# Performance work log

Hardware: AMD Instinct MI355X
Metric: run time of the kernel (lower is better)

The kernel has to match this reference:

```python
import jax, jax.numpy as jnp
import numpy as np

D_MODEL = 1024
N_HEAD = 16
DK = D_MODEL // N_HEAD
D_FF = 2048
EPS = 1e-6
NEG = -1e10


def layer_norm(x, gamma, beta):
    # torch .std() is unbiased (N-1), and eps is added to std (not var)
    mean = jnp.mean(x, axis=-1, keepdims=True)
    var = jnp.sum((x - mean) ** 2, axis=-1, keepdims=True) / (x.shape[-1] - 1)
    std = jnp.sqrt(var)
    return gamma * (x - mean) / (std + EPS) + beta


def setup_inputs() -> dict:
    key = jax.random.key(0)
    ks = jax.random.split(key, 12)
    s = 0.02
    inp = {
        'x': jax.random.normal(ks[0], (16, 512, D_MODEL), dtype=jnp.float32),
        'x_mask': jax.random.randint(ks[1], (16, 1, 1, 512), 0, 2, dtype=jnp.int32),
        'Wq': jax.random.normal(ks[2], (D_MODEL, D_MODEL), dtype=jnp.float32) * s,
        'bq': jnp.zeros((D_MODEL,), jnp.float32),
        'Wk': jax.random.normal(ks[3], (D_MODEL, D_MODEL), dtype=jnp.float32) * s,
        'bk': jnp.zeros((D_MODEL,), jnp.float32),
        'Wv': jax.random.normal(ks[4], (D_MODEL, D_MODEL), dtype=jnp.float32) * s,
        'bv': jnp.zeros((D_MODEL,), jnp.float32),
        'Wo': jax.random.normal(ks[5], (D_MODEL, D_MODEL), dtype=jnp.float32) * s,
        'bo': jnp.zeros((D_MODEL,), jnp.float32),
        'gamma1': jnp.ones((D_MODEL,), jnp.float32),
        'beta1': jnp.zeros((D_MODEL,), jnp.float32),
        'W1': jax.random.normal(ks[6], (D_MODEL, D_FF), dtype=jnp.float32) * s,
        'b1': jnp.zeros((D_FF,), jnp.float32),
        'W2': jax.random.normal(ks[7], (D_FF, D_MODEL), dtype=jnp.float32) * s,
        'b2': jnp.zeros((D_MODEL,), jnp.float32),
        'gamma2': jnp.ones((D_MODEL,), jnp.float32),
        'beta2': jnp.zeros((D_MODEL,), jnp.float32),
    }
    return inp


def reference(x, x_mask, Wq, bq, Wk, bk, Wv, bv, Wo, bo, gamma1, beta1,
              W1, b1, W2, b2, gamma2, beta2):
    B, S, _ = x.shape
    # QKV projections -> [B, S, H, DK]
    q = (x @ Wq + bq).reshape(B, S, N_HEAD, DK)
    k = (x @ Wk + bk).reshape(B, S, N_HEAD, DK)
    v = (x @ Wv + bv).reshape(B, S, N_HEAD, DK)
    # scores [B, H, Sq, Sk]
    scores = jnp.einsum('bqhd,bkhd->bhqk', q, k) / jnp.sqrt(jnp.float32(DK))
    scores = jnp.where(x_mask == 0, jnp.float32(NEG), scores)
    probs = jax.nn.softmax(scores, axis=-1)
    attn = jnp.einsum('bhqk,bkhd->bqhd', probs, v).reshape(B, S, D_MODEL)
    attn_out = attn @ Wo + bo
    # residual + post-LN 1
    h = layer_norm(attn_out + x, gamma1, beta1)
    # FFN (exact GELU as torch nn.GELU default)
    ffn = jax.nn.gelu(h @ W1 + b1, approximate=False) @ W2 + b2
    out = layer_norm(ffn + h, gamma2, beta2)
    return out
```

## Files before the change

### kernel.cpp

```cpp
#include <hip/hip_runtime.h>
#include <math.h>

#define B_ 16
#define S_ 512
#define DM 1024
#define NH 16
#define DFF 2048

typedef short bf16x8 __attribute__((ext_vector_type(8)));
typedef float f32x4 __attribute__((ext_vector_type(4)));
typedef unsigned short u16;

__device__ __forceinline__ u16 f2bf(float f) {
  unsigned int u = __float_as_uint(f);
  u += 0x7FFF + ((u >> 16) & 1);
  return (u16)(u >> 16);
}

__device__ __forceinline__ float gelu_exact(float x) {
  return 0.5f * x * (1.0f + erff(x * 0.70710678118654752f));
}

__device__ __forceinline__ void gload_lds16(const void* g, void* l) {
  __builtin_amdgcn_global_load_lds((const __attribute__((address_space(1))) void*)g,
                                   (__attribute__((address_space(3))) void*)l, 16, 0, 0);
}


__global__ void cvt_bf16_k(const float* __restrict__ in, u16* __restrict__ out, int n) {
  int i = (blockIdx.x * blockDim.x + threadIdx.x) * 4;
  float4 v = *(const float4*)(in + i);
  uint2 pk;
  pk.x = (unsigned)f2bf(v.x) | ((unsigned)f2bf(v.y) << 16);
  pk.y = (unsigned)f2bf(v.z) | ((unsigned)f2bf(v.w) << 16);
  *(uint2*)(out + i) = pk;
}

__global__ void transpose_bf16(const float* __restrict__ W, u16* __restrict__ Wt, int K, int N) {
  __shared__ float tile[32][33];
  int n0 = blockIdx.x * 32, k0 = blockIdx.y * 32;
  int tx = threadIdx.x, ty = threadIdx.y;
#pragma unroll
  for (int j = 0; j < 32; j += 8)
    tile[ty + j][tx] = W[(size_t)(k0 + ty + j) * N + n0 + tx];
  __syncthreads();
#pragma unroll
  for (int j = 0; j < 32; j += 8)
    Wt[(size_t)(n0 + ty + j) * K + k0 + tx] = f2bf(tile[tx][ty + j]);
}

__global__ void bias_cat(const float* __restrict__ bq, const float* __restrict__ bk,
                         const float* __restrict__ bv, float* __restrict__ o) {
  int i = blockIdx.x * 256 + threadIdx.x;
  o[i] = (i < 1024) ? bq[i] : ((i < 2048) ? bk[i - 1024] : bv[i - 2048]);
}

template <int EPI>
__global__ __launch_bounds__(256, 2)
void gemm_mfma(const u16* __restrict__ A, const u16* __restrict__ Bt,
               const float* __restrict__ bias, void* __restrict__ Cout,
               u16* __restrict__ vT, int M, int N, int K) {
  __shared__ __align__(16) char lds[73728];
  const int tid = threadIdx.x;
  const int w = tid >> 6, lane = tid & 63;
  const int wm = w >> 1, wn = w & 1;

  const int gx = gridDim.x;
  const int nwg = gx * gridDim.y;
  const int lin = blockIdx.y * gx + blockIdx.x;
  const int wg = (lin & 7) * (nwg >> 3) + (lin >> 3);
  const int bm = wg / gx, bn = wg % gx;

  const int NT = K >> 5;

  const int srow = w * 16 + (lane >> 2);
  const int skel = ((lane & 3) ^ (lane >> 4)) * 8;
  const u16* gA = A + (size_t)(bm * 256 + srow) * K + skel;
  const u16* gB = Bt + (size_t)(bn * 128 + srow) * K + skel;
  const size_t rs64 = (size_t)64 * K;
  const int dstb = w * 1024;

  const int lr = lane & 15, kg = lane >> 4;
  const int kslot = (kg ^ ((lr >> 2) & 3)) << 4;
  const int fAoff = (wm * 128 + lr) * 64 + kslot;
  const int fBoff = 16384 + (wn * 64 + lr) * 64 + kslot;

  f32x4 acc[8][4];
#pragma unroll
  for (int i = 0; i < 8; ++i)
#pragma unroll
    for (int j = 0; j < 4; ++j) acc[i][j] = (f32x4){0.f, 0.f, 0.f, 0.f};

#define STAGE_A(t_, sl_)                                         \
  do {                                                           \
    const u16* g_ = gA + (size_t)(t_) * 32;                      \
    char* d_ = lds + (sl_) * 24576 + dstb;                       \
    gload_lds16(g_, d_);                                         \
    gload_lds16(g_ + rs64, d_ + 4096);                           \
    gload_lds16(g_ + 2 * rs64, d_ + 8192);                       \
    gload_lds16(g_ + 3 * rs64, d_ + 12288);                      \
  } while (0)
#define STAGE_B(t_, sl_)                                         \
  do {                                                           \
    const u16* g_ = gB + (size_t)(t_) * 32;                      \
    char* d_ = lds + (sl_) * 24576 + 16384 + dstb;               \
    gload_lds16(g_, d_);                                         \
    gload_lds16(g_ + rs64, d_ + 4096);                           \
  } while (0)

  STAGE_A(0, 0);
  STAGE_B(0, 0);
  STAGE_A(1, 1);
  STAGE_B(1, 1);
  asm volatile("s_waitcnt vmcnt(6)" ::: "memory");
  __builtin_amdgcn_s_barrier();
  __builtin_amdgcn_sched_barrier(0);

  int cs = 0, ss = 2;
  for (int t = 0; t < NT; ++t) {
    const int st = (t + 2 < NT) ? (t + 2) : (NT - 1);
    const char* fA = lds + cs * 24576 + fAoff;
    const char* fB = lds + cs * 24576 + fBoff;
    bf16x8 av[4], bv[4];
#pragma unroll
    for (int mi = 0; mi < 4; ++mi) av[mi] = *(const bf16x8*)(fA + mi * 1024);
#pragma unroll
    for (int ni = 0; ni < 4; ++ni) bv[ni] = *(const bf16x8*)(fB + ni * 1024);
    STAGE_A(st, ss);
    __builtin_amdgcn_s_barrier();
    asm volatile("s_waitcnt lgkmcnt(0)" ::: "memory");
    __builtin_amdgcn_sched_barrier(0);
    __builtin_amdgcn_s_setprio(1);
#pragma unroll
    for (int mi = 0; mi < 4; ++mi)
#pragma unroll
      for (int ni = 0; ni < 4; ++ni)
        acc[mi][ni] = __builtin_amdgcn_mfma_f32_16x16x32_bf16(av[mi], bv[ni], acc[mi][ni], 0, 0, 0);
    __builtin_amdgcn_s_setprio(0);
    __builtin_amdgcn_s_barrier();
    __builtin_amdgcn_sched_barrier(0);
#pragma unroll
    for (int mi = 0; mi < 4; ++mi) av[mi] = *(const bf16x8*)(fA + 4096 + mi * 1024);
    STAGE_B(st, ss);
    __builtin_amdgcn_s_barrier();
    asm volatile("s_waitcnt lgkmcnt(0)" ::: "memory");
    __builtin_amdgcn_sched_barrier(0);
    __builtin_amdgcn_s_setprio(1);
#pragma unroll
    for (int mi = 0; mi < 4; ++mi)
#pragma unroll
      for (int ni = 0; ni < 4; ++ni)
        acc[4 + mi][ni] = __builtin_amdgcn_mfma_f32_16x16x32_bf16(av[mi], bv[ni], acc[4 + mi][ni], 0, 0, 0);
    __builtin_amdgcn_s_setprio(0);
    asm volatile("s_waitcnt vmcnt(6)" ::: "memory");
    __builtin_amdgcn_s_barrier();
    __builtin_amdgcn_sched_barrier(0);
    cs = (cs == 2) ? 0 : cs + 1;
    ss = (ss == 2) ? 0 : ss + 1;
  }
#undef STAGE_A
#undef STAGE_B

  const int crow0 = bm * 256 + wm * 128;
  const int ccol0 = bn * 128 + wn * 64;
#pragma unroll
  for (int mi = 0; mi < 8; ++mi) {
#pragma unroll
    for (int ni = 0; ni < 4; ++ni) {
      const int col = ccol0 + ni * 16 + lr;
      const float bv = bias[col];
      const int rowb = crow0 + mi * 16 + (lane >> 4) * 4;
      float v[4];
#pragma unroll
      for (int r = 0; r < 4; ++r) v[r] = acc[mi][ni][r] + bv;
      if (EPI == 1) {
#pragma unroll
        for (int r = 0; r < 4; ++r)
          ((u16*)Cout)[(size_t)(rowb + r) * N + col] = f2bf(gelu_exact(v[r]));
      } else if (EPI == 2) {
#pragma unroll
        for (int r = 0; r < 4; ++r)
          ((float*)Cout)[(size_t)(rowb + r) * N + col] = v[r];
      } else {
        if (col < 2048) {
#pragma unroll
          for (int r = 0; r < 4; ++r)
            ((u16*)Cout)[(size_t)(rowb + r) * 2048 + col] = f2bf(v[r]);
        } else {
          const int b = rowb >> 9, s = rowb & 511;
          const int hd = col - 2048;
          ushort4 pk;
          pk.x = f2bf(v[0]); pk.y = f2bf(v[1]); pk.z = f2bf(v[2]); pk.w = f2bf(v[3]);
          *(ushort4*)(vT + ((size_t)(b * NH + (hd >> 6)) * 64 + (hd & 63)) * S_ + s) = pk;
        }
      }
    }
  }
}

__global__ __launch_bounds__(256, 3)
void attn_kernel(const u16* __restrict__ qk,
                 const u16* __restrict__ vT,
                 const int* __restrict__ mask,
                 u16* __restrict__ out) {
  __shared__ __align__(16) u16 Qs[32 * 72];
  __shared__ __align__(16) u16 Pl[32 * 520];
  __shared__ int Ml[512];
  __shared__ __align__(16) float Rmax[32][4];
  __shared__ __align__(16) float Rsum[32][4];

  const int tid = threadIdx.x;
  const int w = tid >> 6, lane = tid & 63;
  const int bid = blockIdx.x;
  const int widx = (bid & 7) * 512 + (bid >> 3);
  const int qt = widx & 15, h = (widx >> 4) & 15, b = widx >> 8;
  const int q0 = qt * 32;
  const int arow = lane & 15, kg = lane >> 4;

  {
    int r = tid >> 3, slot = tid & 7;
    bf16x8 v = *(const bf16x8*)(qk + (size_t)(b * S_ + q0 + r) * 2048 + h * 64 + slot * 8);
    *(bf16x8*)((char*)Qs + r * 144 + slot * 16) = v;
  }
  Ml[tid] = mask[b * S_ + tid];
  Ml[tid + 256] = mask[b * S_ + tid + 256];
  __syncthreads();

  f32x4 s0[8], s1[8];
  {
    bf16x8 af[2][2];
#pragma unroll
    for (int mi = 0; mi < 2; ++mi)
#pragma unroll
      for (int kk = 0; kk < 2; ++kk)
        af[mi][kk] = *(const bf16x8*)((char*)Qs + (mi * 16 + arow) * 144 + kk * 64 + kg * 16);
    const u16* kbase = qk + (size_t)(b * S_) * 2048 + 1024 + h * 64;
#pragma unroll
    for (int ni = 0; ni < 8; ++ni) {
      const int colg = w * 128 + ni * 16 + arow;
      const u16* kr = kbase + (size_t)colg * 2048 + kg * 8;
      bf16x8 bk0 = *(const bf16x8*)(kr);
      bf16x8 bk1 = *(const bf16x8*)(kr + 32);
      f32x4 a0 = {0.f, 0.f, 0.f, 0.f}, a1 = {0.f, 0.f, 0.f, 0.f};
      a0 = __builtin_amdgcn_mfma_f32_16x16x32_bf16(af[0][0], bk0, a0, 0, 0, 0);
      a0 = __builtin_amdgcn_mfma_f32_16x16x32_bf16(af[0][1], bk1, a0, 0, 0, 0);
      a1 = __builtin_amdgcn_mfma_f32_16x16x32_bf16(af[1][0], bk0, a1, 0, 0, 0);
      a1 = __builtin_amdgcn_mfma_f32_16x16x32_bf16(af[1][1], bk1, a1, 0, 0, 0);
      const bool msk = (Ml[colg] == 0);
#pragma unroll
      for (int r = 0; r < 4; ++r) {
        s0[ni][r] = msk ? -1e10f : a0[r] * 0.125f;
        s1[ni][r] = msk ? -1e10f : a1[r] * 0.125f;
      }
    }
  }

  float m0[4], m1[4];
#pragma unroll
  for (int r = 0; r < 4; ++r) {
    float a = fmaxf(fmaxf(s0[0][r], s0[1][r]), fmaxf(s0[2][r], s0[3][r]));
    float c = fmaxf(fmaxf(s0[4][r], s0[5][r]), fmaxf(s0[6][r], s0[7][r]));
    m0[r] = fmaxf(a, c);
    a = fmaxf(fmaxf(s1[0][r], s1[1][r]), fmaxf(s1[2][r], s1[3][r]));
    c = fmaxf(fmaxf(s1[4][r], s1[5][r]), fmaxf(s1[6][r], s1[7][r]));
    m1[r] = fmaxf(a, c);
  }
#pragma unroll
  for (int d = 1; d < 16; d <<= 1) {
#pragma unroll
    for (int r = 0; r < 4; ++r) {
      m0[r] = fmaxf(m0[r], __shfl_xor(m0[r], d));
      m1[r] = fmaxf(m1[r], __shfl_xor(m1[r], d));
    }
  }
  if (arow == 0) {
#pragma unroll
    for (int r = 0; r < 4; ++r) {
      Rmax[kg * 4 + r][w] = m0[r];
      Rmax[16 + kg * 4 + r][w] = m1[r];
    }
  }
  __syncthreads();
  float fm0[4], fm1[4];
#pragma unroll
  for (int r = 0; r < 4; ++r) {
    f32x4 v = *(const f32x4*)&Rmax[kg * 4 + r][0];
    fm0[r] = fmaxf(fmaxf(v[0], v[1]), fmaxf(v[2], v[3]));
    v = *(const f32x4*)&Rmax[16 + kg * 4 + r][0];
    fm1[r] = fmaxf(fmaxf(v[0], v[1]), fmaxf(v[2], v[3]));
  }

  float t0[4] = {0.f, 0.f, 0.f, 0.f}, t1[4] = {0.f, 0.f, 0.f, 0.f};
#pragma unroll
  for (int ni = 0; ni < 8; ++ni) {
#pragma unroll
    for (int r = 0; r < 4; ++r) {
      s0[ni][r] = __expf(s0[ni][r] - fm0[r]);
      t0[r] += s0[ni][r];
      s1[ni][r] = __expf(s1[ni][r] - fm1[r]);
      t1[r] += s1[ni][r];
    }
  }
#pragma unroll
  for (int ni = 0; ni < 8; ++ni) {
    const int colg = w * 128 + ni * 16 + arow;
#pragma unroll
    for (int r = 0; r < 4; ++r) {
      Pl[(kg * 4 + r) * 520 + colg] = f2bf(s0[ni][r]);
      Pl[(16 + kg * 4 + r) * 520 + colg] = f2bf(s1[ni][r]);
    }
  }
#pragma unroll
  for (int d = 1; d < 16; d <<= 1) {
#pragma unroll
    for (int r = 0; r < 4; ++r) {
      t0[r] += __shfl_xor(t0[r], d);
      t1[r] += __shfl_xor(t1[r], d);
    }
  }
  if (arow == 0) {
#pragma unroll
    for (int r = 0; r < 4; ++r) {
      Rsum[kg * 4 + r][w] = t0[r];
      Rsum[16 + kg * 4 + r][w] = t1[r];
    }
  }
  __syncthreads();

  {
    f32x4 oa[2];
    oa[0] = (f32x4){0.f, 0.f, 0.f, 0.f};
    oa[1] = (f32x4){0.f, 0.f, 0.f, 0.f};
    const u16* vb = vT + ((size_t)(b * NH + h) * 64 + w * 16 + arow) * S_ + kg * 8;
#pragma unroll
    for (int t16 = 0; t16 < 16; ++t16) {
      const int sk0 = t16 * 32;
      bf16x8 bfr = *(const bf16x8*)(vb + sk0);
#pragma unroll
      for (int mi = 0; mi < 2; ++mi) {
        bf16x8 pa = *(const bf16x8*)(Pl + (mi * 16 + arow) * 520 + sk0 + kg * 8);
        oa[mi] = __builtin_amdgcn_mfma_f32_16x16x32_bf16(pa, bfr, oa[mi], 0, 0, 0);
      }
    }
#pragma unroll
    for (int mi = 0; mi < 2; ++mi)
#pragma unroll
      for (int r = 0; r < 4; ++r) {
        const int rloc = mi * 16 + kg * 4 + r;
        f32x4 sv = *(const f32x4*)&Rsum[rloc][0];
        const float inv = 1.0f / (sv[0] + sv[1] + sv[2] + sv[3]);
        const int qrow = q0 + rloc;
        out[(size_t)(b * S_ + qrow) * DM + h * 64 + w * 16 + arow] = f2bf(oa[mi][r] * inv);
      }
  }
}

__global__ __launch_bounds__(256)
void ln_kernel(const float* __restrict__ a, const float* __restrict__ res,
               const float* __restrict__ gamma, const float* __restrict__ beta,
               float* __restrict__ out, u16* __restrict__ outb) {
  const int row = blockIdx.x, tid = threadIdx.x;
  const int w = tid >> 6, lane = tid & 63;
  const size_t base = (size_t)row * DM + tid * 4;
  float4 va = *(const float4*)(a + base);
  float4 vr = *(const float4*)(res + base);
  float v0 = va.x + vr.x, v1 = va.y + vr.y, v2 = va.z + vr.z, v3 = va.w + vr.w;
  float s = v0 + v1 + v2 + v3;
  float ss = v0 * v0 + v1 * v1 + v2 * v2 + v3 * v3;
#pragma unroll
  for (int off = 32; off >= 1; off >>= 1) {
    s += __shfl_down(s, off);
    ss += __shfl_down(ss, off);
  }
  __shared__ float ps[4], pss[4], mb[2];
  if (lane == 0) { ps[w] = s; pss[w] = ss; }
  __syncthreads();
  if (tid == 0) {
    float S = ps[0] + ps[1] + ps[2] + ps[3];
    float SS = pss[0] + pss[1] + pss[2] + pss[3];
    float mean = S * (1.0f / DM);
    float var = (SS - (float)DM * mean * mean) * (1.0f / (DM - 1));
    var = fmaxf(var, 0.f);
    mb[0] = mean;
    mb[1] = 1.0f / (sqrtf(var) + 1e-6f);
  }
  __syncthreads();
  const float mean = mb[0], rinv = mb[1];
  const int c = tid * 4;
  float y0 = gamma[c] * (v0 - mean) * rinv + beta[c];
  float y1 = gamma[c + 1] * (v1 - mean) * rinv + beta[c + 1];
  float y2 = gamma[c + 2] * (v2 - mean) * rinv + beta[c + 2];
  float y3 = gamma[c + 3] * (v3 - mean) * rinv + beta[c + 3];
  float4 o = {y0, y1, y2, y3};
  *(float4*)(out + base) = o;
  if (outb) {
    uint2 pk;
    pk.x = (unsigned)f2bf(y0) | ((unsigned)f2bf(y1) << 16);
    pk.y = (unsigned)f2bf(y2) | ((unsigned)f2bf(y3) << 16);
    *(uint2*)(outb + base) = pk;
  }
}


extern "C" void kernel_launch(void* const* d_in, const int* in_sizes, int n_in,
                              void* d_out, int out_size, void* d_ws, size_t ws_size,
                              hipStream_t stream) {
  const float* x = (const float*)d_in[0];
  const int* xm = (const int*)d_in[1];
  const float* Wq = (const float*)d_in[2];
  const float* bq = (const float*)d_in[3];
  const float* Wk = (const float*)d_in[4];
  const float* bk = (const float*)d_in[5];
  const float* Wv = (const float*)d_in[6];
  const float* bv = (const float*)d_in[7];
  const float* Wo = (const float*)d_in[8];
  const float* bo = (const float*)d_in[9];
  const float* g1 = (const float*)d_in[10];
  const float* be1 = (const float*)d_in[11];
  const float* W1 = (const float*)d_in[12];
  const float* b1 = (const float*)d_in[13];
  const float* W2 = (const float*)d_in[14];
  const float* b2 = (const float*)d_in[15];
  const float* g2 = (const float*)d_in[16];
  const float* be2 = (const float*)d_in[17];

  char* ws = (char*)d_ws;
  u16* xb = (u16*)(ws);
  u16* wqkvt = (u16*)(ws + 16777216);
  u16* wot = (u16*)(ws + 23068672);
  u16* w1t = (u16*)(ws + 25165824);
  u16* w2t = (u16*)(ws + 29360128);
  float* bqkv = (float*)(ws + 33554432);
  u16* qkb = (u16*)(ws + 33566720);
  u16* vtb = (u16*)(ws + 67121152);
  u16* attnb = (u16*)(ws + 83898368);
  float* f32a = (float*)(ws + 100675584);
  float* hbuf = (float*)(ws + 134230016);
  u16* hb = xb;

  cvt_bf16_k<<<dim3(8192), dim3(256), 0, stream>>>(x, xb, 8388608);
  transpose_bf16<<<dim3(32, 32), dim3(32, 8), 0, stream>>>(Wq, wqkvt, 1024, 1024);
  transpose_bf16<<<dim3(32, 32), dim3(32, 8), 0, stream>>>(Wk, wqkvt + 1024 * 1024, 1024, 1024);
  transpose_bf16<<<dim3(32, 32), dim3(32, 8), 0, stream>>>(Wv, wqkvt + 2 * 1024 * 1024, 1024, 1024);
  transpose_bf16<<<dim3(32, 32), dim3(32, 8), 0, stream>>>(Wo, wot, 1024, 1024);
  transpose_bf16<<<dim3(64, 32), dim3(32, 8), 0, stream>>>(W1, w1t, 1024, 2048);
  transpose_bf16<<<dim3(32, 64), dim3(32, 8), 0, stream>>>(W2, w2t, 2048, 1024);
  bias_cat<<<dim3(12), dim3(256), 0, stream>>>(bq, bk, bv, bqkv);

  gemm_mfma<3><<<dim3(24, 32), dim3(256), 0, stream>>>(xb, wqkvt, bqkv, (void*)qkb, vtb, 8192, 3072, 1024);
  attn_kernel<<<dim3(4096), dim3(256), 0, stream>>>(qkb, vtb, xm, attnb);
  gemm_mfma<2><<<dim3(8, 32), dim3(256), 0, stream>>>(attnb, wot, bo, (void*)f32a, (u16*)nullptr, 8192, 1024, 1024);
  ln_kernel<<<dim3(8192), dim3(256), 0, stream>>>(f32a, x, g1, be1, hbuf, hb);
  gemm_mfma<1><<<dim3(16, 32), dim3(256), 0, stream>>>(hb, w1t, b1, (void*)qkb, (u16*)nullptr, 8192, 2048, 1024);
  gemm_mfma<2><<<dim3(8, 32), dim3(256), 0, stream>>>(qkb, w2t, b2, (void*)f32a, (u16*)nullptr, 8192, 1024, 2048);
  ln_kernel<<<dim3(8192), dim3(256), 0, stream>>>(f32a, hbuf, g2, be2, (float*)d_out, (u16*)nullptr);
}
```

Measured before the change: 322.8 us.

## Transpose score MFMA, fold softmax scale into Q, use exp2 and packed bf16 stores

```diff
diff --git a/kernel.cpp b/kernel.cpp
--- a/kernel.cpp
+++ b/kernel.cpp
@@ -17,6 +17,12 @@
   return (u16)(u >> 16);
 }
 
+__device__ __forceinline__ unsigned cvtpk_bf16(float lo, float hi) {
+  unsigned r;
+  asm("v_cvt_pk_bf16_f32 %0, %1, %2" : "=v"(r) : "v"(lo), "v"(hi));
+  return r;
+}
+
 __device__ __forceinline__ float gelu_exact(float x) {
   return 0.5f * x * (1.0f + erff(x * 0.70710678118654752f));
 }
@@ -25,6 +31,9 @@
   __builtin_amdgcn_global_load_lds((const __attribute__((address_space(1))) void*)g,
                                    (__attribute__((address_space(3))) void*)l, 16, 0, 0);
 }
+
+#define QSCALE 0.18033688011112042f
+#define MASKNEG -1.442695e10f
 
 
 __global__ void cvt_bf16_k(const float* __restrict__ in, u16* __restrict__ out, int n) {
@@ -183,9 +192,10 @@
           ((float*)Cout)[(size_t)(rowb + r) * N + col] = v[r];
       } else {
         if (col < 2048) {
+          const float sc = (col < 1024) ? QSCALE : 1.0f;
 #pragma unroll
           for (int r = 0; r < 4; ++r)
-            ((u16*)Cout)[(size_t)(rowb + r) * 2048 + col] = f2bf(v[r]);
+            ((u16*)Cout)[(size_t)(rowb + r) * 2048 + col] = f2bf(v[r] * sc);
         } else {
           const int b = rowb >> 9, s = rowb & 511;
           const int hd = col - 2048;
@@ -205,7 +215,7 @@
                  u16* __restrict__ out) {
   __shared__ __align__(16) u16 Qs[32 * 72];
   __shared__ __align__(16) u16 Pl[32 * 520];
-  __shared__ int Ml[512];
+  __shared__ __align__(16) float Mlf[512];
   __shared__ __align__(16) float Rmax[32][4];
   __shared__ __align__(16) float Rsum[32][4];
 
@@ -222,18 +232,21 @@
     bf16x8 v = *(const bf16x8*)(qk + (size_t)(b * S_ + q0 + r) * 2048 + h * 64 + slot * 8);
     *(bf16x8*)((char*)Qs + r * 144 + slot * 16) = v;
   }
-  Ml[tid] = mask[b * S_ + tid];
-  Ml[tid + 256] = mask[b * S_ + tid + 256];
-  __syncthreads();
+  Mlf[tid] = (mask[b * S_ + tid] == 0) ? MASKNEG : 0.f;
+  Mlf[tid + 256] = (mask[b * S_ + tid + 256] == 0) ? MASKNEG : 0.f;
+  __syncthreads();
+
+  bf16x8 qf[2][2];
+#pragma unroll
+  for (int mi = 0; mi < 2; ++mi)
+#pragma unroll
+    for (int kk = 0; kk < 2; ++kk)
+      qf[mi][kk] = *(const bf16x8*)((char*)Qs + (mi * 16 + arow) * 144 + kk * 64 + kg * 16);
 
   f32x4 s0[8], s1[8];
+  f32x4 vm0 = {-3.0e38f, -3.0e38f, -3.0e38f, -3.0e38f};
+  f32x4 vm1 = vm0;
   {
-    bf16x8 af[2][2];
-#pragma unroll
-    for (int mi = 0; mi < 2; ++mi)
-#pragma unroll
-      for (int kk = 0; kk < 2; ++kk)
-        af[mi][kk] = *(const bf16x8*)((char*)Qs + (mi * 16 + arow) * 144 + kk * 64 + kg * 16);
     const u16* kbase = qk + (size_t)(b * S_) * 2048 + 1024 + h * 64;
 #pragma unroll
     for (int ni = 0; ni < 8; ++ni) {
@@ -242,87 +255,75 @@
       bf16x8 bk0 = *(const bf16x8*)(kr);
       bf16x8 bk1 = *(const bf16x8*)(kr + 32);
       f32x4 a0 = {0.f, 0.f, 0.f, 0.f}, a1 = {0.f, 0.f, 0.f, 0.f};
-      a0 = __builtin_amdgcn_mfma_f32_16x16x32_bf16(af[0][0], bk0, a0, 0, 0, 0);
-      a0 = __builtin_amdgcn_mfma_f32_16x16x32_bf16(af[0][1], bk1, a0, 0, 0, 0);
-      a1 = __builtin_amdgcn_mfma_f32_16x16x32_bf16(af[1][0], bk0, a1, 0, 0, 0);
-      a1 = __builtin_amdgcn_mfma_f32_16x16x32_bf16(af[1][1], bk1, a1, 0, 0, 0);
-      const bool msk = (Ml[colg] == 0);
+      a0 = __builtin_amdgcn_mfma_f32_16x16x32_bf16(bk0, qf[0][0], a0, 0, 0, 0);
+      a0 = __builtin_amdgcn_mfma_f32_16x16x32_bf16(bk1, qf[0][1], a0, 0, 0, 0);
+      a1 = __builtin_amdgcn_mfma_f32_16x16x32_bf16(bk0, qf[1][0], a1, 0, 0, 0);
+      a1 = __builtin_amdgcn_mfma_f32_16x16x32_bf16(bk1, qf[1][1], a1, 0, 0, 0);
+      const f32x4 mb = *(const f32x4*)&Mlf[w * 128 + ni * 16 + kg * 4];
+      s0[ni] = a0 + mb;
+      s1[ni] = a1 + mb;
 #pragma unroll
       for (int r = 0; r < 4; ++r) {
-        s0[ni][r] = msk ? -1e10f : a0[r] * 0.125f;
-        s1[ni][r] = msk ? -1e10f : a1[r] * 0.125f;
+        vm0[r] = fmaxf(vm0[r], s0[ni][r]);
+        vm1[r] = fmaxf(vm1[r], s1[ni][r]);
       }
     }
   }
 
-  float m0[4], m1[4];
-#pragma unroll
-  for (int r = 0; r < 4; ++r) {
-    float a = fmaxf(fmaxf(s0[0][r], s0[1][r]), fmaxf(s0[2][r], s0[3][r]));
-    float c = fmaxf(fmaxf(s0[4][r], s0[5][r]), fmaxf(s0[6][r], s0[7][r]));
-    m0[r] = fmaxf(a, c);
-    a = fmaxf(fmaxf(s1[0][r], s1[1][r]), fmaxf(s1[2][r], s1[3][r]));
-    c = fmaxf(fmaxf(s1[4][r], s1[5][r]), fmaxf(s1[6][r], s1[7][r]));
-    m1[r] = fmaxf(a, c);
-  }
-#pragma unroll
-  for (int d = 1; d < 16; d <<= 1) {
+  float m0 = fmaxf(fmaxf(vm0[0], vm0[1]), fmaxf(vm0[2], vm0[3]));
+  float m1 = fmaxf(fmaxf(vm1[0], vm1[1]), fmaxf(vm1[2], vm1[3]));
+  m0 = fmaxf(m0, __shfl_xor(m0, 16));
+  m0 = fmaxf(m0, __shfl_xor(m0, 32));
+  m1 = fmaxf(m1, __shfl_xor(m1, 16));
+  m1 = fmaxf(m1, __shfl_xor(m1, 32));
+  if (kg == 0) {
+    Rmax[arow][w] = m0;
+    Rmax[16 + arow][w] = m1;
+  }
+  __syncthreads();
+  float fm0, fm1;
+  {
+    f32x4 v = *(const f32x4*)&Rmax[arow][0];
+    fm0 = fmaxf(fmaxf(v[0], v[1]), fmaxf(v[2], v[3]));
+    v = *(const f32x4*)&Rmax[16 + arow][0];
+    fm1 = fmaxf(fmaxf(v[0], v[1]), fmaxf(v[2], v[3]));
+  }
+
+  f32x4 ac0 = {0.f, 0.f, 0.f, 0.f}, ac1 = ac0;
+#pragma unroll
+  for (int ni = 0; ni < 8; ++ni) {
 #pragma unroll
     for (int r = 0; r < 4; ++r) {
-      m0[r] = fmaxf(m0[r], __shfl_xor(m0[r], d));
-      m1[r] = fmaxf(m1[r], __shfl_xor(m1[r], d));
+      s0[ni][r] = __builtin_amdgcn_exp2f(s0[ni][r] - fm0);
+      s1[ni][r] = __builtin_amdgcn_exp2f(s1[ni][r] - fm1);
     }
-  }
-  if (arow == 0) {
-#pragma unroll
-    for (int r = 0; r < 4; ++r) {
-      Rmax[kg * 4 + r][w] = m0[r];
-      Rmax[16 + kg * 4 + r][w] = m1[r];
-    }
-  }
-  __syncthreads();
-  float fm0[4], fm1[4];
-#pragma unroll
-  for (int r = 0; r < 4; ++r) {
-    f32x4 v = *(const f32x4*)&Rmax[kg * 4 + r][0];
-    fm0[r] = fmaxf(fmaxf(v[0], v[1]), fmaxf(v[2], v[3]));
-    v = *(const f32x4*)&Rmax[16 + kg * 4 + r][0];
-    fm1[r] = fmaxf(fmaxf(v[0], v[1]), fmaxf(v[2], v[3]));
-  }
-
-  float t0[4] = {0.f, 0.f, 0.f, 0.f}, t1[4] = {0.f, 0.f, 0.f, 0.f};
-#pragma unroll
-  for (int ni = 0; ni < 8; ++ni) {
-#pragma unroll
-    for (int r = 0; r < 4; ++r) {
-      s0[ni][r] = __expf(s0[ni][r] - fm0[r]);
-      t0[r] += s0[ni][r];
-      s1[ni][r] = __expf(s1[ni][r] - fm1[r]);
-      t1[r] += s1[ni][r];
-    }
-  }
-#pragma unroll
-  for (int ni = 0; ni < 8; ++ni) {
-    const int colg = w * 128 + ni * 16 + arow;
-#pragma unroll
-    for (int r = 0; r < 4; ++r) {
-      Pl[(kg * 4 + r) * 520 + colg] = f2bf(s0[ni][r]);
-      Pl[(16 + kg * 4 + r) * 520 + colg] = f2bf(s1[ni][r]);
-    }
-  }
-#pragma unroll
-  for (int d = 1; d < 16; d <<= 1) {
-#pragma unroll
-    for (int r = 0; r < 4; ++r) {
-      t0[r] += __shfl_xor(t0[r], d);
-      t1[r] += __shfl_xor(t1[r], d);
-    }
-  }
-  if (arow == 0) {
-#pragma unroll
-    for (int r = 0; r < 4; ++r) {
-      Rsum[kg * 4 + r][w] = t0[r];
-      Rsum[16 + kg * 4 + r][w] = t1[r];
+    ac0 += s0[ni];
+    ac1 += s1[ni];
+  }
+  float t0 = ac0[0] + ac0[1] + ac0[2] + ac0[3];
+  float t1 = ac1[0] + ac1[1] + ac1[2] + ac1[3];
+  t0 += __shfl_xor(t0, 16);
+  t0 += __shfl_xor(t0, 32);
+  t1 += __shfl_xor(t1, 16);
+  t1 += __shfl_xor(t1, 32);
+  if (kg == 0) {
+    Rsum[arow][w] = t0;
+    Rsum[16 + arow][w] = t1;
+  }
+
+  {
+    const int kq = w * 128 + kg * 4;
+    char* const p0 = (char*)Pl + (arow * 520 + kq) * 2;
+    char* const p1 = (char*)Pl + ((16 + arow) * 520 + kq) * 2;
+#pragma unroll
+    for (int ni = 0; ni < 8; ++ni) {
+      uint2 pk;
+      pk.x = cvtpk_bf16(s0[ni][0], s0[ni][1]);
+      pk.y = cvtpk_bf16(s0[ni][2], s0[ni][3]);
+      *(uint2*)(p0 + ni * 32) = pk;
+      pk.x = cvtpk_bf16(s1[ni][0], s1[ni][1]);
+      pk.y = cvtpk_bf16(s1[ni][2], s1[ni][3]);
+      *(uint2*)(p1 + ni * 32) = pk;
     }
   }
   __syncthreads();
```

Result: no change. 320.3 us (-0.8%).
